# Optimization experiments

Measured on AMD Instinct MI355X. Metric: run time of the kernel, lower is better.

The kernel has to match this reference:

```python
import jax, jax.numpy as jnp
import numpy as np

L, C, B = 256, 20, 1024


def _pos_mask(L):
    # pairwise mask: l2 - l1 >= 1, shape (L, L); broadcast over channels
    ls = jnp.arange(L)
    return (ls[None, :] - ls[:, None]) >= 1


def setup_inputs() -> dict:
    key = jax.random.key(0)
    k0, k1, k2 = jax.random.split(key, 3)
    x_lc = jax.random.uniform(k0, (B, L, C), dtype=jnp.float32)
    theta_0 = jnp.zeros((1,), dtype=jnp.float32)
    theta_lc = jax.random.normal(k1, (1, L, C), dtype=jnp.float32) / np.sqrt(L)
    pm = _pos_mask(L)
    theta_lclc = (jax.random.normal(k2, (1, L, C, L, C), dtype=jnp.float32)
                  / np.sqrt(L * L)) * pm[None, :, None, :, None]
    mask = pm
    return {"x_lc": x_lc, "theta_0": theta_0, "theta_lc": theta_lc,
            "theta_lclc": theta_lclc, "mask": mask}


def reference(x_lc, theta_0, theta_lc, theta_lclc, mask):
    Bn = x_lc.shape[0]
    # additive term: sum_{l,c} theta_lc * x
    phi = theta_0 + jnp.einsum('blc,zlc->b', x_lc, theta_lc)[:, None]
    # pairwise term as a masked bilinear form: x^T (mask * theta) x
    # (avoids materializing the (B,L,C,L,C) broadcast of the original)
    theta_m = theta_lclc[0] * mask[:, None, :, None].astype(theta_lclc.dtype)
    LC = L * C
    xf = x_lc.reshape(Bn, LC)                      # (B, LC)
    tf_ = theta_m.reshape(LC, LC)                  # (LC, LC)
    pair = jnp.einsum('bi,ij,bj->b', xf, tf_, xf)  # two GEMMs under the hood
    phi = phi + pair[:, None]
    return phi
```

## Files before the change

### kernel.cpp

```cpp
#include <hip/hip_runtime.h>
#include <stdint.h>

#define LDIM 256
#define CDIM 20
#define LC   5120
#define NB   1024
#define BM   128
#define BN   256
#define ITOT64 1640

typedef __attribute__((ext_vector_type(8))) short short8;
typedef __attribute__((ext_vector_type(4))) float float4v;
typedef __attribute__((ext_vector_type(4))) unsigned int uint4v;
typedef unsigned short ushort_t;

#define XB_BYTES (10485760ull)
#define WS_NEED  (XB_BYTES)

__device__ inline uint32_t pack_bf16x2(float a, float b) {
    uint32_t ua = __float_as_uint(a);
    uint32_t ub = __float_as_uint(b);
    ua += 0x7fffu + ((ua >> 16) & 1u);
    ub += 0x7fffu + ((ub >> 16) & 1u);
    return (ua >> 16) | (ub & 0xffff0000u);
}

__device__ inline float bf16_to_f32(ushort_t u) {
    return __uint_as_float(((uint32_t)u) << 16);
}

__device__ inline void load_lds16(const void* g, void* l) {
    __builtin_amdgcn_global_load_lds(
        (const __attribute__((address_space(1))) uint32_t*)g,
        (__attribute__((address_space(3))) uint32_t*)l, 16, 0, 0);
}

__global__ __launch_bounds__(256) void xconv_kernel(
    const float* __restrict__ X, const float* __restrict__ th0,
    const float* __restrict__ thlc, ushort_t* __restrict__ Xb,
    float* __restrict__ out)
{
    const int b = blockIdx.x;
    const int t = threadIdx.x;
    __shared__ float red[4];

    const float*  src = X  + (size_t)b * LC;
    ushort_t*     dst = Xb + (size_t)b * LC;
    float s = 0.f;
    for (int c = t * 4; c < LC; c += 1024) {
        float4 f = *(const float4*)(src + c);
        float4 w = *(const float4*)(thlc + c);
        s += f.x * w.x + f.y * w.y + f.z * w.z + f.w * w.w;
        uint2 u;
        u.x = pack_bf16x2(f.x, f.y);
        u.y = pack_bf16x2(f.z, f.w);
        *(uint2*)(dst + c) = u;
    }
    s += __shfl_xor(s, 1);  s += __shfl_xor(s, 2);  s += __shfl_xor(s, 4);
    s += __shfl_xor(s, 8);  s += __shfl_xor(s, 16); s += __shfl_xor(s, 32);
    if ((t & 63) == 0) red[t >> 6] = s;
    __syncthreads();
    if (t == 0) out[b] = th0[0] + red[0] + red[1] + red[2] + red[3];
}

__global__ __launch_bounds__(256, 2) void pair_fused(
    const float* __restrict__ T, const ushort_t* __restrict__ Xb,
    float* __restrict__ out)
{
    const int n    = blockIdx.x;
    const int kblk = ((n >> 3) << 1) | (n & 1);
    const int bn0  = ((n >> 1) & 3) * BN;

    const int gbeg = (ITOT64 * kblk) >> 7;
    const int gend = (ITOT64 * (kblk + 1)) >> 7;

    int it = 0, pre = 0;
    while (pre + (80 - 2 * it) <= gbeg) { pre += 80 - 2 * it; ++it; }
    int li = gbeg - pre;

    __shared__ __align__(16) ushort_t A_s[1024 * 8];
    __shared__ __align__(16) ushort_t B_s[2048 * 8];

    const int t    = threadIdx.x;
    const int lane = t & 63;
    const int wid  = t >> 6;
    const int wm   = (wid >> 1) * 64;
    const int wn   = (wid & 1) * 128;
    const int l16  = lane & 15;
    const int qk   = lane >> 4;

    const int r32 = t >> 3;
    const int ga  = t & 7;
    uint32_t offTa[4];
    int      wAdr[4];
    #pragma unroll
    for (int j = 0; j < 4; ++j) {
        const int row = r32 + j * 32;
        offTa[j] = (uint32_t)row * LC + (ga << 3);
        wAdr[j]  = ((row << 3) + (ga ^ (row & 7))) << 4;
    }

    uint32_t offB[8];
    #pragma unroll
    for (int j = 0; j < 8; ++j) {
        const int c = (wid << 9) + (j << 6) + lane;
        const int row = c >> 3;
        const int g = (c & 7) ^ (row & 7);
        offB[j] = (uint32_t)(bn0 + row) * LC + (g << 3);
    }

    int adrA[2][4], adrB[2][8];
    #pragma unroll
    for (int step = 0; step < 2; ++step) {
        const int kf = step * 4 + qk;
        #pragma unroll
        for (int mt = 0; mt < 4; ++mt) {
            const int r = wm + mt * 16 + l16;
            adrA[step][mt] = ((r << 3) + (kf ^ (r & 7))) << 4;
        }
        #pragma unroll
        for (int nt = 0; nt < 8; ++nt) {
            const int r = wn + nt * 16 + l16;
            adrB[step][nt] = ((r << 3) + (kf ^ (r & 7))) << 4;
        }
    }

    int i0 = it << 7;
    int k0 = i0 + (li << 6);

    float4v acc[4][8];
    #pragma unroll
    for (int mt = 0; mt < 4; ++mt)
        #pragma unroll
        for (int nt = 0; nt < 8; ++nt)
            #pragma unroll
            for (int r = 0; r < 4; ++r) acc[mt][nt][r] = 0.f;

    for (int g = gbeg; g < gend; ++g) {
        __syncthreads();

        const float* Tbase = T + (size_t)i0 * LC + k0;
        float4 a0[4], a1[4];
        #pragma unroll
        for (int j = 0; j < 4; ++j) {
            a0[j] = *(const float4*)(Tbase + offTa[j]);
            a1[j] = *(const float4*)(Tbase + offTa[j] + 4);
        }
        #pragma unroll
        for (int j = 0; j < 8; ++j)
            load_lds16(Xb + k0 + offB[j], B_s + (((wid << 9) + (j << 6)) << 3));
        #pragma unroll
        for (int j = 0; j < 4; ++j) {
            uint4v v;
            v[0] = pack_bf16x2(a0[j].x, a0[j].y);
            v[1] = pack_bf16x2(a0[j].z, a0[j].w);
            v[2] = pack_bf16x2(a1[j].x, a1[j].y);
            v[3] = pack_bf16x2(a1[j].z, a1[j].w);
            *(uint4v*)((char*)A_s + wAdr[j]) = v;
        }
        __syncthreads();

        #pragma unroll
        for (int step = 0; step < 2; ++step) {
            short8 af[4], bfr[8];
            #pragma unroll
            for (int mt = 0; mt < 4; ++mt)
                af[mt] = *(const short8*)((const char*)A_s + adrA[step][mt]);
            #pragma unroll
            for (int nt = 0; nt < 8; ++nt)
                bfr[nt] = *(const short8*)((const char*)B_s + adrB[step][nt]);
            #pragma unroll
            for (int mt = 0; mt < 4; ++mt)
                #pragma unroll
                for (int nt = 0; nt < 8; ++nt)
                    acc[mt][nt] = __builtin_amdgcn_mfma_f32_16x16x32_bf16(
                        af[mt], bfr[nt], acc[mt][nt], 0, 0, 0);
        }

        ++li;
        const bool segEnd = (li == 80 - 2 * it);
        if (segEnd || g + 1 == gend) {
            #pragma unroll
            for (int nt = 0; nt < 8; ++nt) {
                const int b = bn0 + wn + nt * 16 + l16;
                const ushort_t* xb = Xb + (size_t)b * LC + i0 + wm + qk * 4;
                float s = 0.f;
                #pragma unroll
                for (int mt = 0; mt < 4; ++mt) {
                    ushort4 xv = *(const ushort4*)(xb + mt * 16);
                    s += acc[mt][nt][0] * bf16_to_f32(xv.x)
                       + acc[mt][nt][1] * bf16_to_f32(xv.y)
                       + acc[mt][nt][2] * bf16_to_f32(xv.z)
                       + acc[mt][nt][3] * bf16_to_f32(xv.w);
                }
                s += __shfl_xor(s, 16);
                s += __shfl_xor(s, 32);
                if (qk == 0) atomicAdd(&out[b], s);
            }
            #pragma unroll
            for (int mt = 0; mt < 4; ++mt)
                #pragma unroll
                for (int nt = 0; nt < 8; ++nt)
                    #pragma unroll
                    for (int r = 0; r < 4; ++r) acc[mt][nt][r] = 0.f;
        }
        if (segEnd) {
            ++it; li = 0;
            if (it < 40) {
                i0 = it << 7;
                k0 = i0;
            }
        } else {
            k0 += 64;
        }
    }
}

__global__ __launch_bounds__(256) void init_kernel(
    const float* __restrict__ x, const float* __restrict__ th0,
    const float* __restrict__ thlc, float* __restrict__ out)
{
    const int b = blockIdx.x;
    const float4* xb = (const float4*)(x + (size_t)b * LC);
    const float4* tv = (const float4*)thlc;
    float s = 0.f;
    for (int i = threadIdx.x; i < LC / 4; i += 256) {
        float4 a = xb[i], t = tv[i];
        s += a.x * t.x + a.y * t.y + a.z * t.z + a.w * t.w;
    }
    s += __shfl_xor(s, 1);  s += __shfl_xor(s, 2);  s += __shfl_xor(s, 4);
    s += __shfl_xor(s, 8);  s += __shfl_xor(s, 16); s += __shfl_xor(s, 32);
    __shared__ float red[4];
    if ((threadIdx.x & 63) == 0) red[threadIdx.x >> 6] = s;
    __syncthreads();
    if (threadIdx.x == 0) out[b] = th0[0] + red[0] + red[1] + red[2] + red[3];
}

__global__ __launch_bounds__(256) void pair_kernel(
    const float* __restrict__ T, const float* __restrict__ X,
    float* __restrict__ out)
{
    const int n  = blockIdx.x;
    const int r  = n & 7;
    const int g  = n >> 3;
    const int i0  = (g >> 3) * BM;
    const int bn0 = (g & 7) * 128;
    const int kstart = i0;
    const int nIter  = (LC - kstart) >> 6;
    const int ipc    = (nIter + 7) >> 3;
    const int itBeg  = r * ipc;
    const int itEnd  = (itBeg + ipc < nIter) ? (itBeg + ipc) : nIter;
    if (itBeg >= itEnd) return;
    const int kbeg   = kstart + (itBeg << 6);

    __shared__ __align__(16) short A_s[8 * BM * 8];
    __shared__ __align__(16) short B_s[8 * BM * 8];

    const int t    = threadIdx.x;
    const int lane = t & 63;
    const int wid  = t >> 6;
    const int wm   = (wid >> 1) * 64;
    const int wn   = (wid & 1) * 64;
    const int l16  = lane & 15;
    const int qk   = lane >> 4;

    const float* pA[4]; const float* pB[4]; int sIdx[4];
    #pragma unroll
    for (int u = 0; u < 4; ++u) {
        const int id  = t + u * 256;
        const int row = id >> 3;
        const int kq  = id & 7;
        pA[u] = T + (size_t)(i0 + row) * LC + kbeg + kq * 8;
        pB[u] = X + (size_t)(bn0 + row) * LC + kbeg + kq * 8;
        sIdx[u] = (kq * BM + (row ^ kq)) * 8;
    }

    float4v acc[4][4] = {};
    for (int itr = itBeg; itr < itEnd; ++itr) {
        __syncthreads();
        #pragma unroll
        for (int u = 0; u < 4; ++u) {
            float4 a0 = ((const float4*)pA[u])[0];
            float4 a1 = ((const float4*)pA[u])[1];
            float4 b0 = ((const float4*)pB[u])[0];
            float4 b1 = ((const float4*)pB[u])[1];
            pA[u] += 64; pB[u] += 64;
            uint4v va, vb;
            va[0] = pack_bf16x2(a0.x, a0.y); va[1] = pack_bf16x2(a0.z, a0.w);
            va[2] = pack_bf16x2(a1.x, a1.y); va[3] = pack_bf16x2(a1.z, a1.w);
            vb[0] = pack_bf16x2(b0.x, b0.y); vb[1] = pack_bf16x2(b0.z, b0.w);
            vb[2] = pack_bf16x2(b1.x, b1.y); vb[3] = pack_bf16x2(b1.z, b1.w);
            *(uint4v*)(A_s + sIdx[u]) = va;
            *(uint4v*)(B_s + sIdx[u]) = vb;
        }
        __syncthreads();
        #pragma unroll
        for (int step = 0; step < 2; ++step) {
            const int kf = step * 4 + qk;
            short8 af[4], bfr[4];
            #pragma unroll
            for (int mt = 0; mt < 4; ++mt)
                af[mt] = *(const short8*)(A_s + (kf * BM + ((wm + mt * 16 + l16) ^ kf)) * 8);
            #pragma unroll
            for (int nt = 0; nt < 4; ++nt)
                bfr[nt] = *(const short8*)(B_s + (kf * BM + ((wn + nt * 16 + l16) ^ kf)) * 8);
            #pragma unroll
            for (int mt = 0; mt < 4; ++mt)
                #pragma unroll
                for (int nt = 0; nt < 4; ++nt)
                    acc[mt][nt] = __builtin_amdgcn_mfma_f32_16x16x32_bf16(
                        af[mt], bfr[nt], acc[mt][nt], 0, 0, 0);
        }
    }
    #pragma unroll
    for (int nt = 0; nt < 4; ++nt) {
        const int b = bn0 + wn + nt * 16 + l16;
        const float* xb = X + (size_t)b * LC + i0 + wm + qk * 4;
        float s = 0.f;
        #pragma unroll
        for (int mt = 0; mt < 4; ++mt) {
            float4 xv = *(const float4*)(xb + mt * 16);
            s += acc[mt][nt][0] * xv.x + acc[mt][nt][1] * xv.y +
                 acc[mt][nt][2] * xv.z + acc[mt][nt][3] * xv.w;
        }
        s += __shfl_xor(s, 16);
        s += __shfl_xor(s, 32);
        if (qk == 0) atomicAdd(&out[b], s);
    }
}

extern "C" void kernel_launch(void* const* d_in, const int* in_sizes, int n_in,
                              void* d_out, int out_size, void* d_ws, size_t ws_size,
                              hipStream_t stream) {
    const float* x    = (const float*)d_in[0];
    const float* th0  = (const float*)d_in[1];
    const float* thlc = (const float*)d_in[2];
    const float* T    = (const float*)d_in[3];
    float* out = (float*)d_out;

    if (ws_size >= WS_NEED) {
        ushort_t* Xb = (ushort_t*)d_ws;
        xconv_kernel<<<NB, 256, 0, stream>>>(x, th0, thlc, Xb, out);
        pair_fused<<<512, 256, 0, stream>>>(T, Xb, out);
    } else {
        init_kernel<<<NB, 256, 0, stream>>>(x, th0, thlc, out);
        pair_kernel<<<(LC / BM) * (NB / 128) * 8, 256, 0, stream>>>(T, x, out);
    }
}
```

Before: 207.7 us.

## Double-buffer B tile and prefetch next T tile during MFMA compute

Restructures the main GEMM loop into a software pipeline. The X tile now has two LDS buffers. The next iteration's global loads (T into registers, X straight to LDS) are issued before the current tile's MFMAs, and the waits use explicit vmcnt and lgkmcnt counts so only the older loads must finish. The bf16 conversion and A_s store for the next tile happen after the compute barrier. MFMA sections also raise wave priority with s_setprio. The cost is more LDS, which can limit occupancy, more live registers, and hand-counted waitcnt values that must match the number of loads issued.

After: 251.8 us. +21.3%, slower.

```diff
diff --git a/kernel.cpp b/kernel.cpp
--- a/kernel.cpp
+++ b/kernel.cpp
@@ -79,7 +79,7 @@
     int li = gbeg - pre;
 
     __shared__ __align__(16) ushort_t A_s[1024 * 8];
-    __shared__ __align__(16) ushort_t B_s[2048 * 8];
+    __shared__ __align__(16) ushort_t B_s[2][2048 * 8];
 
     const int t    = threadIdx.x;
     const int lane = t & 63;
@@ -105,8 +105,8 @@
     for (int j = 0; j < 8; ++j) {
         const int c = (wid << 9) + (j << 6) + lane;
         const int row = c >> 3;
-        const int g = (c & 7) ^ (row & 7);
-        offB[j] = (uint32_t)(bn0 + row) * LC + (g << 3);
+        const int g2 = (c & 7) ^ (row & 7);
+        offB[j] = (uint32_t)(bn0 + row) * LC + (g2 << 3);
     }
 
     int adrA[2][4], adrB[2][8];
@@ -136,30 +136,60 @@
             #pragma unroll
             for (int r = 0; r < 4; ++r) acc[mt][nt][r] = 0.f;
 
-    for (int g = gbeg; g < gend; ++g) {
-        __syncthreads();
-
-        const float* Tbase = T + (size_t)i0 * LC + k0;
-        float4 a0[4], a1[4];
+    {
+        const float* Tb0 = T + (size_t)i0 * LC + k0;
+        float4 p0[4], p1[4];
         #pragma unroll
         for (int j = 0; j < 4; ++j) {
-            a0[j] = *(const float4*)(Tbase + offTa[j]);
-            a1[j] = *(const float4*)(Tbase + offTa[j] + 4);
+            p0[j] = *(const float4*)(Tb0 + offTa[j]);
+            p1[j] = *(const float4*)(Tb0 + offTa[j] + 4);
         }
         #pragma unroll
         for (int j = 0; j < 8; ++j)
-            load_lds16(Xb + k0 + offB[j], B_s + (((wid << 9) + (j << 6)) << 3));
+            load_lds16(Xb + k0 + offB[j], &B_s[0][(((wid << 9) + (j << 6)) << 3)]);
         #pragma unroll
         for (int j = 0; j < 4; ++j) {
             uint4v v;
-            v[0] = pack_bf16x2(a0[j].x, a0[j].y);
-            v[1] = pack_bf16x2(a0[j].z, a0[j].w);
-            v[2] = pack_bf16x2(a1[j].x, a1[j].y);
-            v[3] = pack_bf16x2(a1[j].z, a1[j].w);
+            v[0] = pack_bf16x2(p0[j].x, p0[j].y);
+            v[1] = pack_bf16x2(p0[j].z, p0[j].w);
+            v[2] = pack_bf16x2(p1[j].x, p1[j].y);
+            v[3] = pack_bf16x2(p1[j].z, p1[j].w);
             *(uint4v*)((char*)A_s + wAdr[j]) = v;
         }
-        __syncthreads();
-
+    }
+
+    int cur = 0;
+    float4 a0[4], a1[4];
+
+    for (int g = gbeg; g < gend; ++g) {
+        const bool haveNext = (g + 1 < gend);
+        const int  li_n   = li + 1;
+        const bool segEnd = (li_n == 80 - 2 * it);
+        const int  it_n   = segEnd ? it + 1 : it;
+        const int  i0_n   = it_n << 7;
+        const int  k0_n   = segEnd ? i0_n : (k0 + 64);
+
+        if (haveNext) {
+            const float* Tb2 = T + (size_t)i0_n * LC + k0_n;
+            #pragma unroll
+            for (int j = 0; j < 4; ++j) {
+                a0[j] = *(const float4*)(Tb2 + offTa[j]);
+                a1[j] = *(const float4*)(Tb2 + offTa[j] + 4);
+            }
+            #pragma unroll
+            for (int j = 0; j < 8; ++j)
+                load_lds16(Xb + k0_n + offB[j],
+                           &B_s[cur ^ 1][(((wid << 9) + (j << 6)) << 3)]);
+        }
+        __builtin_amdgcn_sched_barrier(0);
+        if (haveNext)
+            asm volatile("s_waitcnt vmcnt(16) lgkmcnt(0)" ::: "memory");
+        else
+            asm volatile("s_waitcnt vmcnt(0) lgkmcnt(0)" ::: "memory");
+        __builtin_amdgcn_s_barrier();
+        __builtin_amdgcn_sched_barrier(0);
+
+        const char* Bbase = (const char*)B_s[cur];
         #pragma unroll
         for (int step = 0; step < 2; ++step) {
             short8 af[4], bfr[8];
@@ -168,18 +198,34 @@
                 af[mt] = *(const short8*)((const char*)A_s + adrA[step][mt]);
             #pragma unroll
             for (int nt = 0; nt < 8; ++nt)
-                bfr[nt] = *(const short8*)((const char*)B_s + adrB[step][nt]);
+                bfr[nt] = *(const short8*)(Bbase + adrB[step][nt]);
+            __builtin_amdgcn_s_setprio(1);
             #pragma unroll
             for (int mt = 0; mt < 4; ++mt)
                 #pragma unroll
                 for (int nt = 0; nt < 8; ++nt)
                     acc[mt][nt] = __builtin_amdgcn_mfma_f32_16x16x32_bf16(
                         af[mt], bfr[nt], acc[mt][nt], 0, 0, 0);
-        }
-
-        ++li;
-        const bool segEnd = (li == 80 - 2 * it);
-        if (segEnd || g + 1 == gend) {
+            __builtin_amdgcn_s_setprio(0);
+        }
+
+        __builtin_amdgcn_sched_barrier(0);
+        __builtin_amdgcn_s_barrier();
+        __builtin_amdgcn_sched_barrier(0);
+
+        if (haveNext) {
+            #pragma unroll
+            for (int j = 0; j < 4; ++j) {
+                uint4v v;
+                v[0] = pack_bf16x2(a0[j].x, a0[j].y);
+                v[1] = pack_bf16x2(a0[j].z, a0[j].w);
+                v[2] = pack_bf16x2(a1[j].x, a1[j].y);
+                v[3] = pack_bf16x2(a1[j].z, a1[j].w);
+                *(uint4v*)((char*)A_s + wAdr[j]) = v;
+            }
+        }
+
+        if (segEnd || !haveNext) {
             #pragma unroll
             for (int nt = 0; nt < 8; ++nt) {
                 const int b = bn0 + wn + nt * 16 + l16;
@@ -204,15 +250,12 @@
                     #pragma unroll
                     for (int r = 0; r < 4; ++r) acc[mt][nt][r] = 0.f;
         }
-        if (segEnd) {
-            ++it; li = 0;
-            if (it < 40) {
-                i0 = it << 7;
-                k0 = i0;
-            }
-        } else {
-            k0 += 64;
-        }
+
+        li = segEnd ? 0 : li_n;
+        it = it_n;
+        i0 = i0_n;
+        k0 = k0_n;
+        cur ^= 1;
     }
 }
 
```
